# Kernel optimization log

Hardware: AMD Instinct MI355X
Metric: run time of the kernel (lower is better)

Reference implementation:

```python
import jax, jax.numpy as jnp
import numpy as np

N_NODES = 50000
N_EDGES = 800000
IN_DIM = 128
ATT_DIM = 128
NEG_SLOPE = 0.01  # nn.LeakyReLU default


def setup_inputs() -> dict:
    key = jax.random.key(0)
    ks = jax.random.split(key, 8)
    x = jax.random.normal(ks[0], (N_NODES, IN_DIM), dtype=jnp.float32)
    src_idx = jax.random.randint(ks[1], (N_EDGES,), 0, N_NODES, dtype=jnp.int32)
    dst_idx = jax.random.randint(ks[2], (N_EDGES,), 0, N_NODES, dtype=jnp.int32)
    # small init scale keeps exp(score) numerically tame
    src_w = jax.random.normal(ks[3], (IN_DIM, ATT_DIM), dtype=jnp.float32) * 0.05
    src_b = jnp.zeros((ATT_DIM,), dtype=jnp.float32)
    dst_w = jax.random.normal(ks[4], (IN_DIM, ATT_DIM), dtype=jnp.float32) * 0.05
    dst_b = jnp.zeros((ATT_DIM,), dtype=jnp.float32)
    att_w = jax.random.normal(ks[5], (ATT_DIM, 1), dtype=jnp.float32) * 0.05
    att_b = jnp.zeros((1,), dtype=jnp.float32)
    return {"x": x, "src_idx": src_idx, "dst_idx": dst_idx,
            "src_w": src_w, "src_b": src_b, "dst_w": dst_w, "dst_b": dst_b,
            "att_w": att_w, "att_b": att_b}


def reference(x, src_idx, dst_idx, src_w, src_b, dst_w, dst_b, att_w, att_b):
    n = x.shape[0]
    # 1) mean aggregation of source features onto destinations (copy_u + mean)
    deg = jax.ops.segment_sum(jnp.ones_like(dst_idx, dtype=x.dtype), dst_idx, num_segments=n)
    h_mean = jax.ops.segment_sum(x[src_idx], dst_idx, num_segments=n)
    h_mean = h_mean / jnp.maximum(deg, 1.0)[:, None]
    # 2) attention projections on nodes (dense GEMMs)
    ha_src = x @ src_w + src_b          # [N, att_dim]
    ha_dst = h_mean @ dst_w + dst_b     # [N, att_dim]
    # 3) per-edge u_add_v -> LeakyReLU -> att Linear -> exp
    e = jax.nn.leaky_relu(ha_src[src_idx] + ha_dst[dst_idx], NEG_SLOPE)  # [E, att_dim]
    s = jnp.exp(e @ att_w + att_b)      # [E, 1]
    # 4) edge softmax: normalize by segment sum over destination
    denom = jax.ops.segment_sum(s, dst_idx, num_segments=n)  # [N, 1]
    a = s / denom[dst_idx]              # [E, 1]
    # 5) u_mul_e weighted aggregation (sum)
    out = jax.ops.segment_sum(x[src_idx] * a, dst_idx, num_segments=n)  # [N, in_dim]
    return out
```

## Files before the change

### kernel.cpp

```cpp
#include <hip/hip_runtime.h>
#include <math.h>

#define N_NODES 50000
#define N_EDGES 800000
#define DIM 128
#define NEG_SLOPE 0.01f
#define CAP 64

typedef short v8s __attribute__((ext_vector_type(8)));
typedef float v4f __attribute__((ext_vector_type(4)));

__device__ inline unsigned f2bf2(float a, float b) {
    unsigned ua = __float_as_uint(a);
    unsigned ub = __float_as_uint(b);
    ua = (ua + 0x7fffu + ((ua >> 16) & 1u)) >> 16;
    ub = (ub + 0x7fffu + ((ub >> 16) & 1u)) & 0xffff0000u;
    return ua | ub;
}
__device__ inline float2 bf2f(unsigned u) {
    float2 r;
    r.x = __uint_as_float(u << 16);
    r.y = __uint_as_float(u & 0xffff0000u);
    return r;
}

__global__ __launch_bounds__(256) void k_prepw(
    const float* __restrict__ src_w, const float* __restrict__ dst_w,
    unsigned* __restrict__ whT, int* __restrict__ deg)
{
    int gid = blockIdx.x * 256 + threadIdx.x;
    if (gid < 256 * 64) {
        int n = gid >> 6;
        int kk = gid & 63;
        const float* W = (n < 128) ? src_w : dst_w;
        int col = n & 127;
        float w0 = W[(2 * kk) * DIM + col];
        float w1 = W[(2 * kk + 1) * DIM + col];
        whT[gid] = f2bf2(w0, w1);
    }
    if (gid < N_NODES) deg[gid] = 0;
}

__global__ __launch_bounds__(256) void k_scatter(
    const int* __restrict__ src, const int* __restrict__ dst,
    int* __restrict__ deg, int* __restrict__ slots)
{
    int e = blockIdx.x * 256 + threadIdx.x;
    if (e >= N_EDGES) return;
    int d = dst[e];
    int pos = atomicAdd(&deg[d], 1);
    if (pos < CAP) slots[d * CAP + pos] = src[e] * 64;
}

__global__ __launch_bounds__(256) void k_gemm(
    const float* __restrict__ x, const unsigned* __restrict__ whT,
    const float* __restrict__ src_b, unsigned* __restrict__ hx_u,
    unsigned* __restrict__ yu)
{
    __shared__ unsigned lds[64][196];
    int wave = threadIdx.x >> 6;
    int lane = threadIdx.x & 63;
    int quad = lane >> 4;
    int m = lane & 15;
    int m0 = blockIdx.x * 64 + wave * 16;
    int arow = m0 + m;
    int lr = wave * 16 + m;
    bool live = (arow < N_NODES);

    v8s b[4];
    #pragma unroll
    for (int k0 = 0; k0 < 4; ++k0) {
        float4 f0 = make_float4(0.f, 0.f, 0.f, 0.f);
        float4 f1 = f0;
        if (live) {
            const float4* xp = (const float4*)(x + (size_t)arow * DIM + k0 * 32 + quad * 8);
            f0 = xp[0];
            f1 = xp[1];
        }
        union { unsigned u[4]; v8s s; } pk;
        pk.u[0] = f2bf2(f0.x, f0.y);
        pk.u[1] = f2bf2(f0.z, f0.w);
        pk.u[2] = f2bf2(f1.x, f1.y);
        pk.u[3] = f2bf2(f1.z, f1.w);
        b[k0] = pk.s;
        int c = k0 * 32 + quad * 8 + 1;
        lds[lr][c + 0] = pk.u[0];
        lds[lr][c + 2] = pk.u[1];
        lds[lr][c + 4] = pk.u[2];
        lds[lr][c + 6] = pk.u[3];
    }

    #pragma unroll
    for (int nt = 0; nt < 16; ++nt) {
        v4f acc = {0.f, 0.f, 0.f, 0.f};
        const uint4* ap = (const uint4*)(whT + (size_t)(nt * 16 + m) * 64 + quad * 4);
        #pragma unroll
        for (int k0 = 0; k0 < 4; ++k0) {
            union { uint4 u; v8s s; } af;
            af.u = ap[k0 * 4];
            acc = __builtin_amdgcn_mfma_f32_16x16x32_bf16(af.s, b[k0], acc, 0, 0, 0);
        }
        if (nt < 8) {
            float4 bia = ((const float4*)src_b)[nt * 4 + quad];
            int c = nt * 16 + quad * 4;
            lds[lr][c]     = f2bf2(acc[0] + bia.x, acc[1] + bia.y);
            lds[lr][c + 2] = f2bf2(acc[2] + bia.z, acc[3] + bia.w);
        } else {
            int c = 64 + nt * 8 + quad * 2;
            lds[lr][c]     = f2bf2(acc[0], acc[1]);
            lds[lr][c + 1] = f2bf2(acc[2], acc[3]);
        }
    }
    __syncthreads();

    int rbase = blockIdx.x * 64;
    for (int i = threadIdx.x; i < 64 * 32; i += 256) {
        int r = i >> 5, c = i & 31;
        int row = rbase + r;
        if (row < N_NODES)
            ((uint4*)(hx_u + (size_t)row * 128))[c] = *(const uint4*)&lds[r][c * 4];
    }
    for (int i = threadIdx.x; i < 64 * 16; i += 256) {
        int r = i >> 4, c = i & 15;
        int row = rbase + r;
        if (row < N_NODES)
            ((uint4*)(yu + (size_t)row * 64))[c] = *(const uint4*)&lds[r][128 + c * 4];
    }
}

__global__ __launch_bounds__(256) void k_fuse(
    const uint2* __restrict__ hx, const unsigned* __restrict__ yu,
    const int* __restrict__ slots, const int* __restrict__ deg,
    const float* __restrict__ dst_b, const float* __restrict__ att_w,
    const float* __restrict__ att_b, float* __restrict__ out)
{
    int g = blockIdx.x * 256 + threadIdx.x;
    int node = g >> 6;
    int lane = g & 63;
    int grp = lane >> 4;
    int sl = lane & 15;
    int cnt = deg[node];
    if (cnt == 0) {
        if (grp < 2)
            ((float4*)out)[node * 32 + 2 * sl + grp] = make_float4(0.f, 0.f, 0.f, 0.f);
        return;
    }
    const int* sp = slots + node * CAP;

    float hd[8] = {0.f, 0.f, 0.f, 0.f, 0.f, 0.f, 0.f, 0.f};
    for (int i = grp; i < cnt; i += 4) {
        int off = sp[i];
        uint4 q = *((const uint4*)(yu + off) + sl);
        float2 f;
        f = bf2f(q.x); hd[0] += f.x; hd[1] += f.y;
        f = bf2f(q.y); hd[2] += f.x; hd[3] += f.y;
        f = bf2f(q.z); hd[4] += f.x; hd[5] += f.y;
        f = bf2f(q.w); hd[6] += f.x; hd[7] += f.y;
    }
    float inv = 1.0f / (float)cnt;
    float4 db0 = ((const float4*)dst_b)[2 * sl];
    float4 db1 = ((const float4*)dst_b)[2 * sl + 1];
    #pragma unroll
    for (int j = 0; j < 8; ++j) {
        hd[j] += __shfl_xor(hd[j], 32);
        hd[j] += __shfl_xor(hd[j], 16);
        hd[j] *= inv;
    }
    hd[0] += db0.x; hd[1] += db0.y; hd[2] += db0.z; hd[3] += db0.w;
    hd[4] += db1.x; hd[5] += db1.y; hd[6] += db1.z; hd[7] += db1.w;

    float4 aw0 = ((const float4*)att_w)[2 * sl];
    float4 aw1 = ((const float4*)att_w)[2 * sl + 1];
    float ab = att_b[0];
    float o[8] = {0.f, 0.f, 0.f, 0.f, 0.f, 0.f, 0.f, 0.f};
    float dsum = 0.f;
    for (int i = grp; i < cnt; i += 4) {
        int off = sp[i];
        const uint4* hp = (const uint4*)(hx + off);
        uint4 qa = hp[2 * sl];
        uint4 qb = hp[2 * sl + 1];
        float2 h01 = bf2f(qa.x), h23 = bf2f(qa.z);
        float2 h45 = bf2f(qb.x), h67 = bf2f(qb.z);
        float v, p;
        v = h01.x + hd[0]; v = (v > 0.f) ? v : v * NEG_SLOPE; p  = v * aw0.x;
        v = h01.y + hd[1]; v = (v > 0.f) ? v : v * NEG_SLOPE; p += v * aw0.y;
        v = h23.x + hd[2]; v = (v > 0.f) ? v : v * NEG_SLOPE; p += v * aw0.z;
        v = h23.y + hd[3]; v = (v > 0.f) ? v : v * NEG_SLOPE; p += v * aw0.w;
        v = h45.x + hd[4]; v = (v > 0.f) ? v : v * NEG_SLOPE; p += v * aw1.x;
        v = h45.y + hd[5]; v = (v > 0.f) ? v : v * NEG_SLOPE; p += v * aw1.y;
        v = h67.x + hd[6]; v = (v > 0.f) ? v : v * NEG_SLOPE; p += v * aw1.z;
        v = h67.y + hd[7]; v = (v > 0.f) ? v : v * NEG_SLOPE; p += v * aw1.w;
        p += __shfl_xor(p, 8);
        p += __shfl_xor(p, 4);
        p += __shfl_xor(p, 2);
        p += __shfl_xor(p, 1);
        float s = __expf(p + ab);
        float2 x01 = bf2f(qa.y), x23 = bf2f(qa.w);
        float2 x45 = bf2f(qb.y), x67 = bf2f(qb.w);
        o[0] += s * x01.x; o[1] += s * x01.y;
        o[2] += s * x23.x; o[3] += s * x23.y;
        o[4] += s * x45.x; o[5] += s * x45.y;
        o[6] += s * x67.x; o[7] += s * x67.y;
        dsum += s;
    }
    dsum += __shfl_xor(dsum, 32);
    dsum += __shfl_xor(dsum, 16);
    #pragma unroll
    for (int j = 0; j < 8; ++j) {
        o[j] += __shfl_xor(o[j], 32);
        o[j] += __shfl_xor(o[j], 16);
    }
    float r = 1.0f / dsum;
    if (grp < 2) {
        float4 ov;
        ov.x = o[grp * 4 + 0] * r;
        ov.y = o[grp * 4 + 1] * r;
        ov.z = o[grp * 4 + 2] * r;
        ov.w = o[grp * 4 + 3] * r;
        ((float4*)out)[node * 32 + 2 * sl + grp] = ov;
    }
}

extern "C" void kernel_launch(void* const* d_in, const int* in_sizes, int n_in,
                              void* d_out, int out_size, void* d_ws, size_t ws_size,
                              hipStream_t stream)
{
    const float* x     = (const float*)d_in[0];
    const int*   src   = (const int*)d_in[1];
    const int*   dst   = (const int*)d_in[2];
    const float* src_w = (const float*)d_in[3];
    const float* src_b = (const float*)d_in[4];
    const float* dst_w = (const float*)d_in[5];
    const float* dst_b = (const float*)d_in[6];
    const float* att_w = (const float*)d_in[7];
    const float* att_b = (const float*)d_in[8];
    float* out = (float*)d_out;
    (void)in_sizes; (void)n_in; (void)out_size; (void)ws_size;

    const size_t NF = (size_t)N_NODES * DIM;

    int* ws = (int*)d_ws;
    int* ideg  = ws;
    int* slots = ws + 50048;
    unsigned* whT = (unsigned*)(ws + 3250048);
    unsigned* yu  = whT + 16384;
    uint2*    hx  = (uint2*)(yu + NF / 2);

    k_prepw<<<256, 256, 0, stream>>>(src_w, dst_w, whT, ideg);

    k_scatter<<<N_EDGES / 256, 256, 0, stream>>>(src, dst, ideg, slots);

    k_gemm<<<(N_NODES + 63) / 64, 256, 0, stream>>>(
        x, whT, src_b, (unsigned*)hx, yu);

    k_fuse<<<N_NODES * 64 / 256, 256, 0, stream>>>(
        hx, yu, slots, ideg, dst_b, att_w, att_b, out);
}
```

Before: 257.9 us.

## Merge scatter into GEMM launch and unroll edge loops by two in fuse

The edge scatter kernel is folded into the GEMM kernel as extra blocks, so the atomic slot-building work runs alongside the dense projection instead of as a separate launch. The edge loops in the fused kernel are unrolled by two so more gathers are in flight per iteration. A cap on the per-node count is also added so slots beyond CAP are never read. Scatter blocks reserve the GEMM's large shared memory allocation even though they do not use it, which may limit how many run at once, and unrolling raises register pressure.

```diff
diff --git a/kernel.cpp b/kernel.cpp
--- a/kernel.cpp
+++ b/kernel.cpp
@@ -6,6 +6,8 @@
 #define DIM 128
 #define NEG_SLOPE 0.01f
 #define CAP 64
+#define GB 782
+#define SB 782
 
 typedef short v8s __attribute__((ext_vector_type(8)));
 typedef float v4f __attribute__((ext_vector_type(4)));
@@ -41,23 +43,25 @@
     if (gid < N_NODES) deg[gid] = 0;
 }
 
-__global__ __launch_bounds__(256) void k_scatter(
-    const int* __restrict__ src, const int* __restrict__ dst,
-    int* __restrict__ deg, int* __restrict__ slots)
-{
-    int e = blockIdx.x * 256 + threadIdx.x;
-    if (e >= N_EDGES) return;
-    int d = dst[e];
-    int pos = atomicAdd(&deg[d], 1);
-    if (pos < CAP) slots[d * CAP + pos] = src[e] * 64;
-}
-
-__global__ __launch_bounds__(256) void k_gemm(
+__global__ __launch_bounds__(256) void k_work(
     const float* __restrict__ x, const unsigned* __restrict__ whT,
     const float* __restrict__ src_b, unsigned* __restrict__ hx_u,
-    unsigned* __restrict__ yu)
+    unsigned* __restrict__ yu, const int* __restrict__ src,
+    const int* __restrict__ dst, int* __restrict__ deg,
+    int* __restrict__ slots)
 {
     __shared__ unsigned lds[64][196];
+
+    if (blockIdx.x >= GB) {
+        int tid = (blockIdx.x - GB) * 256 + threadIdx.x;
+        for (int e = tid; e < N_EDGES; e += SB * 256) {
+            int d = dst[e];
+            int pos = atomicAdd(&deg[d], 1);
+            if (pos < CAP) slots[d * CAP + pos] = src[e] * 64;
+        }
+        return;
+    }
+
     int wave = threadIdx.x >> 6;
     int lane = threadIdx.x & 63;
     int quad = lane >> 4;
@@ -145,17 +149,35 @@
             ((float4*)out)[node * 32 + 2 * sl + grp] = make_float4(0.f, 0.f, 0.f, 0.f);
         return;
     }
+    if (cnt > CAP) cnt = CAP;
     const int* sp = slots + node * CAP;
 
     float hd[8] = {0.f, 0.f, 0.f, 0.f, 0.f, 0.f, 0.f, 0.f};
-    for (int i = grp; i < cnt; i += 4) {
-        int off = sp[i];
-        uint4 q = *((const uint4*)(yu + off) + sl);
-        float2 f;
-        f = bf2f(q.x); hd[0] += f.x; hd[1] += f.y;
-        f = bf2f(q.y); hd[2] += f.x; hd[3] += f.y;
-        f = bf2f(q.z); hd[4] += f.x; hd[5] += f.y;
-        f = bf2f(q.w); hd[6] += f.x; hd[7] += f.y;
+    {
+        int i = grp;
+        for (; i + 4 < cnt; i += 8) {
+            int offA = sp[i];
+            int offB = sp[i + 4];
+            uint4 qA = *((const uint4*)(yu + offA) + sl);
+            uint4 qB = *((const uint4*)(yu + offB) + sl);
+            float2 f;
+            f = bf2f(qA.x); hd[0] += f.x; hd[1] += f.y;
+            f = bf2f(qA.y); hd[2] += f.x; hd[3] += f.y;
+            f = bf2f(qA.z); hd[4] += f.x; hd[5] += f.y;
+            f = bf2f(qA.w); hd[6] += f.x; hd[7] += f.y;
+            f = bf2f(qB.x); hd[0] += f.x; hd[1] += f.y;
+            f = bf2f(qB.y); hd[2] += f.x; hd[3] += f.y;
+            f = bf2f(qB.z); hd[4] += f.x; hd[5] += f.y;
+            f = bf2f(qB.w); hd[6] += f.x; hd[7] += f.y;
+        }
+        if (i < cnt) {
+            uint4 q = *((const uint4*)(yu + sp[i]) + sl);
+            float2 f;
+            f = bf2f(q.x); hd[0] += f.x; hd[1] += f.y;
+            f = bf2f(q.y); hd[2] += f.x; hd[3] += f.y;
+            f = bf2f(q.z); hd[4] += f.x; hd[5] += f.y;
+            f = bf2f(q.w); hd[6] += f.x; hd[7] += f.y;
+        }
     }
     float inv = 1.0f / (float)cnt;
     float4 db0 = ((const float4*)dst_b)[2 * sl];
@@ -174,7 +196,60 @@
     float ab = att_b[0];
     float o[8] = {0.f, 0.f, 0.f, 0.f, 0.f, 0.f, 0.f, 0.f};
     float dsum = 0.f;
-    for (int i = grp; i < cnt; i += 4) {
+    int i = grp;
+    for (; i + 4 < cnt; i += 8) {
+        int offA = sp[i];
+        int offB = sp[i + 4];
+        const uint4* hpA = (const uint4*)(hx + offA);
+        const uint4* hpB = (const uint4*)(hx + offB);
+        uint4 qaA = hpA[2 * sl];
+        uint4 qbA = hpA[2 * sl + 1];
+        uint4 qaB = hpB[2 * sl];
+        uint4 qbB = hpB[2 * sl + 1];
+        float2 h01, h23, h45, h67;
+        float v, pA, pB;
+        h01 = bf2f(qaA.x); h23 = bf2f(qaA.z);
+        h45 = bf2f(qbA.x); h67 = bf2f(qbA.z);
+        v = h01.x + hd[0]; v = (v > 0.f) ? v : v * NEG_SLOPE; pA  = v * aw0.x;
+        v = h01.y + hd[1]; v = (v > 0.f) ? v : v * NEG_SLOPE; pA += v * aw0.y;
+        v = h23.x + hd[2]; v = (v > 0.f) ? v : v * NEG_SLOPE; pA += v * aw0.z;
+        v = h23.y + hd[3]; v = (v > 0.f) ? v : v * NEG_SLOPE; pA += v * aw0.w;
+        v = h45.x + hd[4]; v = (v > 0.f) ? v : v * NEG_SLOPE; pA += v * aw1.x;
+        v = h45.y + hd[5]; v = (v > 0.f) ? v : v * NEG_SLOPE; pA += v * aw1.y;
+        v = h67.x + hd[6]; v = (v > 0.f) ? v : v * NEG_SLOPE; pA += v * aw1.z;
+        v = h67.y + hd[7]; v = (v > 0.f) ? v : v * NEG_SLOPE; pA += v * aw1.w;
+        h01 = bf2f(qaB.x); h23 = bf2f(qaB.z);
+        h45 = bf2f(qbB.x); h67 = bf2f(qbB.z);
+        v = h01.x + hd[0]; v = (v > 0.f) ? v : v * NEG_SLOPE; pB  = v * aw0.x;
+        v = h01.y + hd[1]; v = (v > 0.f) ? v : v * NEG_SLOPE; pB += v * aw0.y;
+        v = h23.x + hd[2]; v = (v > 0.f) ? v : v * NEG_SLOPE; pB += v * aw0.z;
+        v = h23.y + hd[3]; v = (v > 0.f) ? v : v * NEG_SLOPE; pB += v * aw0.w;
+        v = h45.x + hd[4]; v = (v > 0.f) ? v : v * NEG_SLOPE; pB += v * aw1.x;
+        v = h45.y + hd[5]; v = (v > 0.f) ? v : v * NEG_SLOPE; pB += v * aw1.y;
+        v = h67.x + hd[6]; v = (v > 0.f) ? v : v * NEG_SLOPE; pB += v * aw1.z;
+        v = h67.y + hd[7]; v = (v > 0.f) ? v : v * NEG_SLOPE; pB += v * aw1.w;
+        pA += __shfl_xor(pA, 8);  pB += __shfl_xor(pB, 8);
+        pA += __shfl_xor(pA, 4);  pB += __shfl_xor(pB, 4);
+        pA += __shfl_xor(pA, 2);  pB += __shfl_xor(pB, 2);
+        pA += __shfl_xor(pA, 1);  pB += __shfl_xor(pB, 1);
+        float sA = __expf(pA + ab);
+        float sB = __expf(pB + ab);
+        float2 x01, x23, x45, x67;
+        x01 = bf2f(qaA.y); x23 = bf2f(qaA.w);
+        x45 = bf2f(qbA.y); x67 = bf2f(qbA.w);
+        o[0] += sA * x01.x; o[1] += sA * x01.y;
+        o[2] += sA * x23.x; o[3] += sA * x23.y;
+        o[4] += sA * x45.x; o[5] += sA * x45.y;
+        o[6] += sA * x67.x; o[7] += sA * x67.y;
+        x01 = bf2f(qaB.y); x23 = bf2f(qaB.w);
+        x45 = bf2f(qbB.y); x67 = bf2f(qbB.w);
+        o[0] += sB * x01.x; o[1] += sB * x01.y;
+        o[2] += sB * x23.x; o[3] += sB * x23.y;
+        o[4] += sB * x45.x; o[5] += sB * x45.y;
+        o[6] += sB * x67.x; o[7] += sB * x67.y;
+        dsum += sA + sB;
+    }
+    if (i < cnt) {
         int off = sp[i];
         const uint4* hp = (const uint4*)(hx + off);
         uint4 qa = hp[2 * sl];
@@ -248,10 +323,8 @@
 
     k_prepw<<<256, 256, 0, stream>>>(src_w, dst_w, whT, ideg);
 
-    k_scatter<<<N_EDGES / 256, 256, 0, stream>>>(src, dst, ideg, slots);
-
-    k_gemm<<<(N_NODES + 63) / 64, 256, 0, stream>>>(
-        x, whT, src_b, (unsigned*)hx, yu);
+    k_work<<<GB + SB, 256, 0, stream>>>(
+        x, whT, src_b, (unsigned*)hx, yu, src, dst, ideg, slots);
 
     k_fuse<<<N_NODES * 64 / 256, 256, 0, stream>>>(
         hx, yu, slots, ideg, dst_b, att_w, att_b, out);
```

Result: slower. 271.9 us (+5.4%).

## Merge edge scatter and node GEMM into one kernel with interleaved block roles

Applied to the files above, without the earlier changes.

Combines the degree/slot scatter kernel and the MFMA projection GEMM into one launch. Odd blocks do the edge scatter with a grid-stride loop and even blocks do the GEMM, so the atomic-bound and compute-bound work can overlap and one launch is saved. The GEMM no longer stages results through LDS and stores them directly to global memory with small strided writes, which removes the barrier but may give less coalesced stores. It also clamps the per-node count to CAP in the fuse kernel so slot reads stay in bounds.

```diff
diff --git a/kernel.cpp b/kernel.cpp
--- a/kernel.cpp
+++ b/kernel.cpp
@@ -6,6 +6,8 @@
 #define DIM 128
 #define NEG_SLOPE 0.01f
 #define CAP 64
+#define GB 782
+#define SB 782
 
 typedef short v8s __attribute__((ext_vector_type(8)));
 typedef float v4f __attribute__((ext_vector_type(4)));
@@ -41,30 +43,30 @@
     if (gid < N_NODES) deg[gid] = 0;
 }
 
-__global__ __launch_bounds__(256) void k_scatter(
-    const int* __restrict__ src, const int* __restrict__ dst,
-    int* __restrict__ deg, int* __restrict__ slots)
-{
-    int e = blockIdx.x * 256 + threadIdx.x;
-    if (e >= N_EDGES) return;
-    int d = dst[e];
-    int pos = atomicAdd(&deg[d], 1);
-    if (pos < CAP) slots[d * CAP + pos] = src[e] * 64;
-}
-
-__global__ __launch_bounds__(256) void k_gemm(
+__global__ __launch_bounds__(256) void k_work(
     const float* __restrict__ x, const unsigned* __restrict__ whT,
     const float* __restrict__ src_b, unsigned* __restrict__ hx_u,
-    unsigned* __restrict__ yu)
-{
-    __shared__ unsigned lds[64][196];
+    unsigned* __restrict__ yu, const int* __restrict__ src,
+    const int* __restrict__ dst, int* __restrict__ deg,
+    int* __restrict__ slots)
+{
+    if (blockIdx.x & 1) {
+        int tid = (blockIdx.x >> 1) * 256 + threadIdx.x;
+        for (int e = tid; e < N_EDGES; e += SB * 256) {
+            int d = dst[e];
+            int pos = atomicAdd(&deg[d], 1);
+            if (pos < CAP) slots[d * CAP + pos] = src[e] * 64;
+        }
+        return;
+    }
+
+    int bid = blockIdx.x >> 1;
     int wave = threadIdx.x >> 6;
     int lane = threadIdx.x & 63;
     int quad = lane >> 4;
     int m = lane & 15;
-    int m0 = blockIdx.x * 64 + wave * 16;
+    int m0 = bid * 64 + wave * 16;
     int arow = m0 + m;
-    int lr = wave * 16 + m;
     bool live = (arow < N_NODES);
 
     v8s b[4];
@@ -83,11 +85,13 @@
         pk.u[2] = f2bf2(f1.x, f1.y);
         pk.u[3] = f2bf2(f1.z, f1.w);
         b[k0] = pk.s;
-        int c = k0 * 32 + quad * 8 + 1;
-        lds[lr][c + 0] = pk.u[0];
-        lds[lr][c + 2] = pk.u[1];
-        lds[lr][c + 4] = pk.u[2];
-        lds[lr][c + 6] = pk.u[3];
+        if (live) {
+            unsigned* hp = hx_u + (size_t)arow * 128 + (k0 * 16 + quad * 4) * 2 + 1;
+            hp[0] = pk.u[0];
+            hp[2] = pk.u[1];
+            hp[4] = pk.u[2];
+            hp[6] = pk.u[3];
+        }
     }
 
     #pragma unroll
@@ -100,31 +104,22 @@
             af.u = ap[k0 * 4];
             acc = __builtin_amdgcn_mfma_f32_16x16x32_bf16(af.s, b[k0], acc, 0, 0, 0);
         }
+        if (!live) continue;
+        int f0v = nt * 16 + quad * 4;
         if (nt < 8) {
             float4 bia = ((const float4*)src_b)[nt * 4 + quad];
-            int c = nt * 16 + quad * 4;
-            lds[lr][c]     = f2bf2(acc[0] + bia.x, acc[1] + bia.y);
-            lds[lr][c + 2] = f2bf2(acc[2] + bia.z, acc[3] + bia.w);
+            unsigned u0 = f2bf2(acc[0] + bia.x, acc[1] + bia.y);
+            unsigned u1 = f2bf2(acc[2] + bia.z, acc[3] + bia.w);
+            unsigned* hp = hx_u + (size_t)arow * 128 + f0v;
+            hp[0] = u0;
+            hp[2] = u1;
         } else {
-            int c = 64 + nt * 8 + quad * 2;
-            lds[lr][c]     = f2bf2(acc[0], acc[1]);
-            lds[lr][c + 1] = f2bf2(acc[2], acc[3]);
-        }
-    }
-    __syncthreads();
-
-    int rbase = blockIdx.x * 64;
-    for (int i = threadIdx.x; i < 64 * 32; i += 256) {
-        int r = i >> 5, c = i & 31;
-        int row = rbase + r;
-        if (row < N_NODES)
-            ((uint4*)(hx_u + (size_t)row * 128))[c] = *(const uint4*)&lds[r][c * 4];
-    }
-    for (int i = threadIdx.x; i < 64 * 16; i += 256) {
-        int r = i >> 4, c = i & 15;
-        int row = rbase + r;
-        if (row < N_NODES)
-            ((uint4*)(yu + (size_t)row * 64))[c] = *(const uint4*)&lds[r][128 + c * 4];
+            int fy = f0v - 128;
+            uint2 u;
+            u.x = f2bf2(acc[0], acc[1]);
+            u.y = f2bf2(acc[2], acc[3]);
+            *(uint2*)(yu + (size_t)arow * 64 + fy / 2) = u;
+        }
     }
 }
 
@@ -145,6 +140,7 @@
             ((float4*)out)[node * 32 + 2 * sl + grp] = make_float4(0.f, 0.f, 0.f, 0.f);
         return;
     }
+    if (cnt > CAP) cnt = CAP;
     const int* sp = slots + node * CAP;
 
     float hd[8] = {0.f, 0.f, 0.f, 0.f, 0.f, 0.f, 0.f, 0.f};
@@ -248,10 +244,8 @@
 
     k_prepw<<<256, 256, 0, stream>>>(src_w, dst_w, whT, ideg);
 
-    k_scatter<<<N_EDGES / 256, 256, 0, stream>>>(src, dst, ideg, slots);
-
-    k_gemm<<<(N_NODES + 63) / 64, 256, 0, stream>>>(
-        x, whT, src_b, (unsigned*)hx, yu);
+    k_work<<<GB + SB, 256, 0, stream>>>(
+        x, whT, src_b, (unsigned*)hx, yu, src, dst, ideg, slots);
 
     k_fuse<<<N_NODES * 64 / 256, 256, 0, stream>>>(
         hx, yu, slots, ideg, dst_b, att_w, att_b, out);
```

New measurement: 258.6 us. About the same (+0.3%).
